# Performance work log

Hardware: AMD Instinct MI355X
Metric: run time of the kernel (lower is better)

## Reference

```python
import jax, jax.numpy as jnp
import numpy as np

CONV1_CH, CONV1_K = 8, 3
CONV2_CH, CONV2_K = 16, 2
DYN_POOL, MAX_POOL = 8, 4
FC1_IN, FC1_OUT = CONV2_CH * MAX_POOL * MAX_POOL, 100  # 256 -> 100


def k_max_pool(x, axis, k):
    # topk along axis, sort indices ascending, gather -> keeps original order of top-k
    xm = jnp.moveaxis(x, axis, -1)
    _, idx = jax.lax.top_k(xm, k)
    idx = jnp.sort(idx, axis=-1)
    out = jnp.take_along_axis(xm, idx, axis=-1)
    return jnp.moveaxis(out, -1, axis)


def _conv2d(x, w, b):
    y = jax.lax.conv_general_dilated(x, w, (1, 1), 'VALID',
                                     dimension_numbers=('NCHW', 'OIHW', 'NCHW'))
    return y + b[None, :, None, None]


def setup_inputs() -> dict:
    key = jax.random.key(0)
    ks = jax.random.split(key, 11)
    Lq, Ld, d, N = 128, 512, 64, 127
    inp = {
        'query': jax.random.normal(ks[0], (Lq, d), jnp.float32),
        'pos_doc': jax.random.normal(ks[1], (Ld, d), jnp.float32),
        'neg_docs': jax.random.normal(ks[2], (N, Ld, d), jnp.float32),
        'conv1_w': jax.random.normal(ks[3], (CONV1_CH, 1, CONV1_K, CONV1_K), jnp.float32) * 0.1,
        'conv1_b': jax.random.normal(ks[4], (CONV1_CH,), jnp.float32) * 0.1,
        'conv2_w': jax.random.normal(ks[5], (CONV2_CH, CONV1_CH, CONV2_K, CONV2_K), jnp.float32) * 0.1,
        'conv2_b': jax.random.normal(ks[6], (CONV2_CH,), jnp.float32) * 0.1,
        'lin1_w': jax.random.normal(ks[7], (FC1_OUT, FC1_IN), jnp.float32) * 0.05,
        'lin1_b': jax.random.normal(ks[8], (FC1_OUT,), jnp.float32) * 0.05,
        'lin2_w': jax.random.normal(ks[9], (1, FC1_OUT), jnp.float32) * 0.05,
        'lin2_b': jax.random.normal(ks[10], (1,), jnp.float32) * 0.05,
    }
    return inp


def reference(query, pos_doc, neg_docs, conv1_w, conv1_b, conv2_w, conv2_b,
              lin1_w, lin1_b, lin2_w, lin2_b):
    # Stack pos doc first, then negs (matches output stacking order in original)
    docs = jnp.concatenate([pos_doc[None], neg_docs], axis=0)      # [B, Ld, d]
    m = jnp.einsum('qd,bld->bql', query, docs)[:, None]            # [B, 1, Lq, Ld]
    # Layer 1: conv + relu + 2D k-max pooling to 8x8
    h = jax.nn.relu(_conv2d(m, conv1_w, conv1_b))                  # [B, 8, Lq-2, Ld-2]
    h = k_max_pool(h, 2, DYN_POOL)
    h = k_max_pool(h, 3, DYN_POOL)                                 # [B, 8, 8, 8]
    # Layer 2: conv + relu + 2D k-max pooling to 4x4
    h = jax.nn.relu(_conv2d(h, conv2_w, conv2_b))                  # [B, 16, 7, 7]
    h = k_max_pool(h, 2, MAX_POOL)
    h = k_max_pool(h, 3, MAX_POOL)                                 # [B, 16, 4, 4]
    feat = h.reshape(h.shape[0], -1)                               # [B, 256]
    z = jax.nn.relu(feat @ lin1_w.T + lin1_b)                      # [B, 100]
    s = jax.nn.relu(z @ lin2_w.T + lin2_b)                         # [B, 1]
    return s
```

## Files before the change

### kernel.cpp

```cpp
#include <hip/hip_runtime.h>
#include <cstdint>
#include <cstddef>

constexpr int kLq = 128;
constexpr int kLd = 512;
constexpr int kD  = 64;
constexpr int kB  = 128;
constexpr int kC1 = 8;
constexpr int kC2 = 16;
constexpr int kH1C = 510;
constexpr int kTileC = 51;
constexpr int kNTiles = 10;
constexpr int kMCols = 53;
constexpr int kNCand = kNTiles * 8;

constexpr int QT_PITCH = 132;
constexpr int DS_PITCH = 68;
constexpr int MS_PITCH = 57;

constexpr int kQtOff = 0;
constexpr int kDsOff = 64 * QT_PITCH;
constexpr int kMsOff = 0;
constexpr int kPsOff = kLq * MS_PITCH;
constexpr int kLdsFloats = kDsOff + 56 * DS_PITCH;

__device__ __forceinline__ uint64_t pack_key(float v, unsigned idx) {
  return ((uint64_t)__float_as_uint(v) << 32) | (uint32_t)(~idx);
}

template <int K>
__device__ __forceinline__ void topk_u64(uint64_t (&key)[K], uint64_t c) {
#pragma unroll
  for (int k = 0; k < K; ++k) {
    const bool g = c > key[k];
    const uint64_t hi = g ? c : key[k];
    c = g ? key[k] : c;
    key[k] = hi;
  }
}

template <int K, bool LEX>
__device__ __forceinline__ void topk_insert(float (&tv)[K], int (&ti)[K],
                                            float v, int idx) {
  bool gK = LEX ? ((v > tv[K - 1]) | ((v == tv[K - 1]) & (idx < ti[K - 1])))
                : (v > tv[K - 1]);
  if (!gK) return;
  bool g[K];
#pragma unroll
  for (int k = 0; k < K; ++k)
    g[k] = LEX ? ((v > tv[k]) | ((v == tv[k]) & (idx < ti[k]))) : (v > tv[k]);
#pragma unroll
  for (int k = K - 1; k >= 1; --k) {
    tv[k] = g[k - 1] ? tv[k - 1] : (g[k] ? v : tv[k]);
    ti[k] = g[k - 1] ? ti[k - 1] : (g[k] ? idx : ti[k]);
  }
  if (g[0]) { tv[0] = v; ti[0] = idx; }
}

__global__ __launch_bounds__(512, 6)
void convpool1_kernel(const float* __restrict__ query,
                      const float* __restrict__ pos_doc,
                      const float* __restrict__ neg_docs,
                      const float* __restrict__ c1w,
                      const float* __restrict__ c1b,
                      float* __restrict__ candv,
                      int* __restrict__ candi) {
  __shared__ float lds[kLdsFloats];
  float* q_t = lds + kQtOff;
  float* d_s = lds + kDsOff;
  float* m_s = lds + kMsOff;
  float* ps  = lds + kPsOff;

  const int tid  = threadIdx.x;
  const int tile = blockIdx.x;
  const int b    = blockIdx.y;
  const int l0g  = tile * kTileC;

  const float* doc =
      (b == 0) ? pos_doc : (neg_docs + (size_t)(b - 1) * kLd * kD);

  {
    const float4* qf4 = reinterpret_cast<const float4*>(query);
    for (int e = tid; e < (kLq * kD) / 4; e += 512) {
      const int q  = e & 127;
      const int f4 = e >> 7;
      const float4 v = qf4[q * 16 + f4];
      const int d0 = f4 << 2;
      q_t[(d0 + 0) * QT_PITCH + q] = v.x;
      q_t[(d0 + 1) * QT_PITCH + q] = v.y;
      q_t[(d0 + 2) * QT_PITCH + q] = v.z;
      q_t[(d0 + 3) * QT_PITCH + q] = v.w;
    }
  }
  for (int e = tid; e < 56 * 16; e += 512) {
    const int l  = e >> 4;
    const int d0 = (e & 15) << 2;
    float4 v = make_float4(0.f, 0.f, 0.f, 0.f);
    if (l < kMCols)
      v = reinterpret_cast<const float4*>(doc + (size_t)(l0g + l) * kD)[e & 15];
    *reinterpret_cast<float4*>(&d_s[l * DS_PITCH + d0]) = v;
  }
  __syncthreads();

  float acc[4][4] = {};
  if (tid < 32 * 14) {
    const int q0 = (tid & 31) << 2;
    const int l0 = (tid >> 5) << 2;
#pragma unroll 4
    for (int d = 0; d < kD; d += 4) {
      float4 qv[4];
#pragma unroll
      for (int j = 0; j < 4; ++j)
        qv[j] = *reinterpret_cast<const float4*>(&q_t[(d + j) * QT_PITCH + q0]);
      float4 dv[4];
#pragma unroll
      for (int li = 0; li < 4; ++li)
        dv[li] = *reinterpret_cast<const float4*>(&d_s[(l0 + li) * DS_PITCH + d]);
#pragma unroll
      for (int li = 0; li < 4; ++li) {
        const float4 w = dv[li];
        acc[0][li] += qv[0].x * w.x + qv[1].x * w.y + qv[2].x * w.z + qv[3].x * w.w;
        acc[1][li] += qv[0].y * w.x + qv[1].y * w.y + qv[2].y * w.z + qv[3].y * w.w;
        acc[2][li] += qv[0].z * w.x + qv[1].z * w.y + qv[2].z * w.z + qv[3].z * w.w;
        acc[3][li] += qv[0].w * w.x + qv[1].w * w.y + qv[2].w * w.z + qv[3].w * w.w;
      }
    }
  }
  __syncthreads();
  if (tid < 32 * 14) {
    const int q0 = (tid & 31) << 2;
    const int l0 = (tid >> 5) << 2;
#pragma unroll
    for (int qi = 0; qi < 4; ++qi)
#pragma unroll
      for (int li = 0; li < 4; ++li)
        m_s[(q0 + qi) * MS_PITCH + (l0 + li)] = acc[qi][li];
  }
  __syncthreads();

  if (tid < kC1 * kTileC) {
    const int c = tid / kTileC;
    const int j = tid % kTileC;
    float w[9];
#pragma unroll
    for (int k = 0; k < 9; ++k) w[k] = c1w[c * 9 + k];
    const float bias = c1b[c];

    uint64_t key[8];
#pragma unroll
    for (int k = 0; k < 8; ++k) key[k] = 0;

    float acc01 = 0.f, s0_pend = 0.f;
    for (int t = 0; t < kLq; ++t) {
      const float x0 = m_s[t * MS_PITCH + j];
      const float x1 = m_s[t * MS_PITCH + j + 1];
      const float x2 = m_s[t * MS_PITCH + j + 2];
      const float S0 = w[0] * x0 + w[1] * x1 + w[2] * x2;
      const float S1 = w[3] * x0 + w[4] * x1 + w[5] * x2;
      const float S2 = w[6] * x0 + w[7] * x1 + w[8] * x2;
      if (t >= 2) {
        const float v = fmaxf(bias + acc01 + S2, 0.f);
        topk_u64<8>(key, pack_key(v, (unsigned)(t - 2)));
      }
      acc01 = s0_pend + S1;
      s0_pend = S0;
    }
#pragma unroll
    for (int k = 0; k < 8; ++k) {
      const uint32_t lo_k = (uint32_t)key[k];
      int slot = 0;
#pragma unroll
      for (int m = 0; m < 8; ++m) slot += ((uint32_t)key[m] > lo_k);
      ps[(c * 8 + slot) * 52 + j] = __uint_as_float((uint32_t)(key[k] >> 32));
    }
  }
  __syncthreads();

  if (tid < 64) {
    const int g = tid;
    uint64_t key[8];
#pragma unroll
    for (int k = 0; k < 8; ++k) key[k] = 0;
    for (int j = 0; j < kTileC; ++j)
      topk_u64<8>(key, pack_key(ps[g * 52 + j], (unsigned)(l0g + j)));
    float* cv = candv + ((size_t)b * 64 + g) * kNCand + tile * 8;
    int*   ci = candi + ((size_t)b * 64 + g) * kNCand + tile * 8;
#pragma unroll
    for (int k = 0; k < 8; ++k) {
      const uint32_t lo_k = (uint32_t)key[k];
      int slot = 0;
#pragma unroll
      for (int m = 0; m < 8; ++m) slot += ((uint32_t)key[m] > lo_k);
      cv[slot] = __uint_as_float((uint32_t)(key[k] >> 32));
      ci[slot] = (int)(~lo_k);
    }
  }
}

__global__ __launch_bounds__(512)
void tail_kernel(const float* __restrict__ candv, const int* __restrict__ candi,
                 const float* __restrict__ c2w, const float* __restrict__ c2b,
                 const float* __restrict__ l1w, const float* __restrict__ l1b,
                 const float* __restrict__ l2w, const float* __restrict__ l2b,
                 float* __restrict__ out) {
  __shared__ float mv[64][8][8];
  __shared__ int   mi[64][8][8];
  __shared__ float w2s[kC2 * kC1 * 4];
  __shared__ float b2s[kC2];
  __shared__ float h2in[kC1][8][8];
  __shared__ float h2o[kC2][7][7];
  __shared__ float h3[kC2][4][7];
  __shared__ __align__(16) float feat[256];
  __shared__ float zbuf[100];

  const int b = blockIdx.x, tid = threadIdx.x;

  if (tid < kC2 * kC1 * 4) w2s[tid] = c2w[tid];
  if (tid < kC2) b2s[tid] = c2b[tid];

  const int g = tid >> 3, lane8 = tid & 7;
  float tv[8]; int ti[8];
#pragma unroll
  for (int k = 0; k < 8; ++k) { tv[k] = -1.f; ti[k] = 0x7fffffff; }
  {
    const float* cv = candv + ((size_t)b * 64 + g) * kNCand;
    const int*   ci = candi + ((size_t)b * 64 + g) * kNCand;
    for (int p = lane8; p < kNCand; p += 8)
      topk_insert<8, false>(tv, ti, cv[p], ci[p]);
#pragma unroll
    for (int k = 0; k < 8; ++k) { mv[g][lane8][k] = tv[k]; mi[g][lane8][k] = ti[k]; }
  }
  __syncthreads();

#pragma unroll
  for (int s = 4; s >= 1; s >>= 1) {
    if (lane8 < s) {
#pragma unroll
      for (int kk = 0; kk < 8; ++kk)
        topk_insert<8, true>(tv, ti, mv[g][lane8 + s][kk], mi[g][lane8 + s][kk]);
      if (s > 1) {
#pragma unroll
        for (int k = 0; k < 8; ++k) { mv[g][lane8][k] = tv[k]; mi[g][lane8][k] = ti[k]; }
      }
    }
    __syncthreads();
  }
  if (lane8 == 0) {
    const int c = g >> 3, row = g & 7;
#pragma unroll
    for (int k = 0; k < 8; ++k) {
      int slot = 0;
#pragma unroll
      for (int m = 0; m < 8; ++m) slot += (ti[m] < ti[k]);
      h2in[c][row][slot] = tv[k];
    }
  }
  __syncthreads();

  for (int v = tid; v < kC2 * 49; v += 512) {
    const int c2 = v / 49;
    const int r  = (v % 49) / 7;
    const int j  = v % 7;
    float s = b2s[c2];
#pragma unroll
    for (int cin = 0; cin < kC1; ++cin) {
      const float* wp = &w2s[(c2 * kC1 + cin) * 4];
      s += wp[0] * h2in[cin][r][j]     + wp[1] * h2in[cin][r][j + 1];
      s += wp[2] * h2in[cin][r + 1][j] + wp[3] * h2in[cin][r + 1][j + 1];
    }
    h2o[c2][r][j] = fmaxf(s, 0.f);
  }
  __syncthreads();

  if (tid < kC2 * 7) {
    const int c2 = tid / 7, j = tid % 7;
    float tv4[4]; int ti4[4];
#pragma unroll
    for (int k = 0; k < 4; ++k) { tv4[k] = -1.f; ti4[k] = 0x7fffffff; }
    for (int r = 0; r < 7; ++r) topk_insert<4, false>(tv4, ti4, h2o[c2][r][j], r);
#pragma unroll
    for (int k = 0; k < 4; ++k) {
      int slot = 0;
#pragma unroll
      for (int m = 0; m < 4; ++m) slot += (ti4[m] < ti4[k]);
      h3[c2][slot][j] = tv4[k];
    }
  }
  __syncthreads();

  if (tid < kC2 * 4) {
    const int c2 = tid >> 2, r = tid & 3;
    float tv4[4]; int ti4[4];
#pragma unroll
    for (int k = 0; k < 4; ++k) { tv4[k] = -1.f; ti4[k] = 0x7fffffff; }
    for (int j = 0; j < 7; ++j) topk_insert<4, false>(tv4, ti4, h3[c2][r][j], j);
#pragma unroll
    for (int k = 0; k < 4; ++k) {
      int slot = 0;
#pragma unroll
      for (int m = 0; m < 4; ++m) slot += (ti4[m] < ti4[k]);
      feat[c2 * 16 + r * 4 + slot] = tv4[k];
    }
  }
  __syncthreads();

  if (tid < 100) {
    const int o = tid;
    float s = l1b[o];
    const float4* wr = reinterpret_cast<const float4*>(l1w + (size_t)o * 256);
    const float4* fr = reinterpret_cast<const float4*>(feat);
    for (int i = 0; i < 64; ++i) {
      const float4 w = wr[i], f = fr[i];
      s += w.x * f.x + w.y * f.y + w.z * f.z + w.w * f.w;
    }
    zbuf[o] = fmaxf(s, 0.f);
  }
  __syncthreads();

  if (tid < 64) {
    float s = 0.f;
    for (int o = tid; o < 100; o += 64) s += zbuf[o] * l2w[o];
#pragma unroll
    for (int off = 32; off >= 1; off >>= 1) s += __shfl_down(s, off, 64);
    if (tid == 0) out[b] = fmaxf(s + l2b[0], 0.f);
  }
}

extern "C" void kernel_launch(void* const* d_in, const int* in_sizes, int n_in,
                              void* d_out, int out_size, void* d_ws,
                              size_t ws_size, hipStream_t stream) {
  const float* query    = (const float*)d_in[0];
  const float* pos_doc  = (const float*)d_in[1];
  const float* neg_docs = (const float*)d_in[2];
  const float* c1w      = (const float*)d_in[3];
  const float* c1b      = (const float*)d_in[4];
  const float* c2w      = (const float*)d_in[5];
  const float* c2b      = (const float*)d_in[6];
  const float* l1w      = (const float*)d_in[7];
  const float* l1b      = (const float*)d_in[8];
  const float* l2w      = (const float*)d_in[9];
  const float* l2b      = (const float*)d_in[10];
  float* out = (float*)d_out;

  float* candv = (float*)d_ws;
  int*   candi = (int*)((char*)d_ws + (size_t)kB * 64 * kNCand * sizeof(float));

  dim3 gridA(kNTiles, kB);
  hipLaunchKernelGGL(convpool1_kernel, gridA, dim3(512), 0, stream,
                     query, pos_doc, neg_docs, c1w, c1b, candv, candi);
  hipLaunchKernelGGL(tail_kernel, dim3(kB), dim3(512), 0, stream,
                     candv, candi, c2w, c2b, l1w, l1b, l2w, l2b, out);
}
```

Baseline: 268.7 us.

## Double block size and split conv1 row scan across thread pairs with LDS merge

The first kernel moves to 1024 threads per block. The matmul now gives each thread 2 query rows instead of 4. The conv1 top-k scan over 128 rows is split between two threads, each handling about half the rows, and their top-8 packed keys are merged through a new LDS buffer. The tail kernel swaps the float/index top-k insertion for packed u64 keys, loads the candidates into registers first, and splits the FC1 dot products across 4 lanes with shuffle reductions. The intent is more parallelism for the serial per-column scan, at the cost of higher register pressure per block, an extra sync, and more LDS use.

After: 273.6 us. No clear change (+1.8%).

```diff
diff --git a/kernel.cpp b/kernel.cpp
--- a/kernel.cpp
+++ b/kernel.cpp
@@ -8,11 +8,11 @@
 constexpr int kB  = 128;
 constexpr int kC1 = 8;
 constexpr int kC2 = 16;
-constexpr int kH1C = 510;
 constexpr int kTileC = 51;
 constexpr int kNTiles = 10;
 constexpr int kMCols = 53;
 constexpr int kNCand = kNTiles * 8;
+constexpr int kNPair = kC1 * kTileC;
 
 constexpr int QT_PITCH = 132;
 constexpr int DS_PITCH = 68;
@@ -21,8 +21,9 @@
 constexpr int kQtOff = 0;
 constexpr int kDsOff = 64 * QT_PITCH;
 constexpr int kMsOff = 0;
-constexpr int kPsOff = kLq * MS_PITCH;
-constexpr int kLdsFloats = kDsOff + 56 * DS_PITCH;
+constexpr int kPsOff = kDsOff;
+constexpr int kHkOff = kDsOff + 56 * DS_PITCH;
+constexpr int kLdsFloats = kHkOff + kNPair * 8 * 2;
 
 __device__ __forceinline__ uint64_t pack_key(float v, unsigned idx) {
   return ((uint64_t)__float_as_uint(v) << 32) | (uint32_t)(~idx);
@@ -39,25 +40,7 @@
   }
 }
 
-template <int K, bool LEX>
-__device__ __forceinline__ void topk_insert(float (&tv)[K], int (&ti)[K],
-                                            float v, int idx) {
-  bool gK = LEX ? ((v > tv[K - 1]) | ((v == tv[K - 1]) & (idx < ti[K - 1])))
-                : (v > tv[K - 1]);
-  if (!gK) return;
-  bool g[K];
-#pragma unroll
-  for (int k = 0; k < K; ++k)
-    g[k] = LEX ? ((v > tv[k]) | ((v == tv[k]) & (idx < ti[k]))) : (v > tv[k]);
-#pragma unroll
-  for (int k = K - 1; k >= 1; --k) {
-    tv[k] = g[k - 1] ? tv[k - 1] : (g[k] ? v : tv[k]);
-    ti[k] = g[k - 1] ? ti[k - 1] : (g[k] ? idx : ti[k]);
-  }
-  if (g[0]) { tv[0] = v; ti[0] = idx; }
-}
-
-__global__ __launch_bounds__(512, 6)
+__global__ __launch_bounds__(1024, 8)
 void convpool1_kernel(const float* __restrict__ query,
                       const float* __restrict__ pos_doc,
                       const float* __restrict__ neg_docs,
@@ -70,6 +53,7 @@
   float* d_s = lds + kDsOff;
   float* m_s = lds + kMsOff;
   float* ps  = lds + kPsOff;
+  uint64_t* hk = reinterpret_cast<uint64_t*>(lds + kHkOff);
 
   const int tid  = threadIdx.x;
   const int tile = blockIdx.x;
@@ -81,7 +65,7 @@
 
   {
     const float4* qf4 = reinterpret_cast<const float4*>(query);
-    for (int e = tid; e < (kLq * kD) / 4; e += 512) {
+    for (int e = tid; e < (kLq * kD) / 4; e += 1024) {
       const int q  = e & 127;
       const int f4 = e >> 7;
       const float4 v = qf4[q * 16 + f4];
@@ -92,26 +76,26 @@
       q_t[(d0 + 3) * QT_PITCH + q] = v.w;
     }
   }
-  for (int e = tid; e < 56 * 16; e += 512) {
-    const int l  = e >> 4;
-    const int d0 = (e & 15) << 2;
+  if (tid < 56 * 16) {
+    const int l  = tid >> 4;
+    const int d0 = (tid & 15) << 2;
     float4 v = make_float4(0.f, 0.f, 0.f, 0.f);
     if (l < kMCols)
-      v = reinterpret_cast<const float4*>(doc + (size_t)(l0g + l) * kD)[e & 15];
+      v = reinterpret_cast<const float4*>(doc + (size_t)(l0g + l) * kD)[tid & 15];
     *reinterpret_cast<float4*>(&d_s[l * DS_PITCH + d0]) = v;
   }
   __syncthreads();
 
-  float acc[4][4] = {};
-  if (tid < 32 * 14) {
-    const int q0 = (tid & 31) << 2;
-    const int l0 = (tid >> 5) << 2;
+  float acc[2][4] = {};
+  if (tid < 64 * 14) {
+    const int q0 = (tid & 63) << 1;
+    const int l0 = (tid >> 6) << 2;
 #pragma unroll 4
     for (int d = 0; d < kD; d += 4) {
-      float4 qv[4];
+      float2 qv[4];
 #pragma unroll
       for (int j = 0; j < 4; ++j)
-        qv[j] = *reinterpret_cast<const float4*>(&q_t[(d + j) * QT_PITCH + q0]);
+        qv[j] = *reinterpret_cast<const float2*>(&q_t[(d + j) * QT_PITCH + q0]);
       float4 dv[4];
 #pragma unroll
       for (int li = 0; li < 4; ++li)
@@ -121,50 +105,63 @@
         const float4 w = dv[li];
         acc[0][li] += qv[0].x * w.x + qv[1].x * w.y + qv[2].x * w.z + qv[3].x * w.w;
         acc[1][li] += qv[0].y * w.x + qv[1].y * w.y + qv[2].y * w.z + qv[3].y * w.w;
-        acc[2][li] += qv[0].z * w.x + qv[1].z * w.y + qv[2].z * w.z + qv[3].z * w.w;
-        acc[3][li] += qv[0].w * w.x + qv[1].w * w.y + qv[2].w * w.z + qv[3].w * w.w;
       }
     }
   }
   __syncthreads();
-  if (tid < 32 * 14) {
-    const int q0 = (tid & 31) << 2;
-    const int l0 = (tid >> 5) << 2;
-#pragma unroll
-    for (int qi = 0; qi < 4; ++qi)
+  if (tid < 64 * 14) {
+    const int q0 = (tid & 63) << 1;
+    const int l0 = (tid >> 6) << 2;
+#pragma unroll
+    for (int qi = 0; qi < 2; ++qi)
 #pragma unroll
       for (int li = 0; li < 4; ++li)
         m_s[(q0 + qi) * MS_PITCH + (l0 + li)] = acc[qi][li];
   }
   __syncthreads();
 
-  if (tid < kC1 * kTileC) {
-    const int c = tid / kTileC;
-    const int j = tid % kTileC;
+  const int h    = tid & 1;
+  const int pair = tid >> 1;
+  uint64_t key[8];
+#pragma unroll
+  for (int k = 0; k < 8; ++k) key[k] = 0;
+  if (pair < kNPair) {
+    const int c = pair / kTileC;
+    const int j = pair % kTileC;
     float w[9];
 #pragma unroll
     for (int k = 0; k < 9; ++k) w[k] = c1w[c * 9 + k];
     const float bias = c1b[c];
-
-    uint64_t key[8];
-#pragma unroll
-    for (int k = 0; k < 8; ++k) key[k] = 0;
+    const int tBase = h ? 63 : 0;
 
     float acc01 = 0.f, s0_pend = 0.f;
-    for (int t = 0; t < kLq; ++t) {
+    for (int s = 0; s < 65; ++s) {
+      const int t = tBase + s;
       const float x0 = m_s[t * MS_PITCH + j];
       const float x1 = m_s[t * MS_PITCH + j + 1];
       const float x2 = m_s[t * MS_PITCH + j + 2];
       const float S0 = w[0] * x0 + w[1] * x1 + w[2] * x2;
       const float S1 = w[3] * x0 + w[4] * x1 + w[5] * x2;
       const float S2 = w[6] * x0 + w[7] * x1 + w[8] * x2;
-      if (t >= 2) {
+      if (s >= 2) {
         const float v = fmaxf(bias + acc01 + S2, 0.f);
         topk_u64<8>(key, pack_key(v, (unsigned)(t - 2)));
       }
       acc01 = s0_pend + S1;
       s0_pend = S0;
     }
+    if (h == 1) {
+#pragma unroll
+      for (int k = 0; k < 8; ++k) hk[pair * 8 + k] = key[k];
+    }
+  }
+  __syncthreads();
+
+  if (pair < kNPair && h == 0) {
+    const int c = pair / kTileC;
+    const int j = pair % kTileC;
+#pragma unroll
+    for (int k = 0; k < 8; ++k) topk_u64<8>(key, hk[pair * 8 + k]);
 #pragma unroll
     for (int k = 0; k < 8; ++k) {
       const uint32_t lo_k = (uint32_t)key[k];
@@ -178,20 +175,20 @@
 
   if (tid < 64) {
     const int g = tid;
-    uint64_t key[8];
-#pragma unroll
-    for (int k = 0; k < 8; ++k) key[k] = 0;
+    uint64_t ck[8];
+#pragma unroll
+    for (int k = 0; k < 8; ++k) ck[k] = 0;
     for (int j = 0; j < kTileC; ++j)
-      topk_u64<8>(key, pack_key(ps[g * 52 + j], (unsigned)(l0g + j)));
+      topk_u64<8>(ck, pack_key(ps[g * 52 + j], (unsigned)(l0g + j)));
     float* cv = candv + ((size_t)b * 64 + g) * kNCand + tile * 8;
     int*   ci = candi + ((size_t)b * 64 + g) * kNCand + tile * 8;
 #pragma unroll
     for (int k = 0; k < 8; ++k) {
-      const uint32_t lo_k = (uint32_t)key[k];
-      int slot = 0;
-#pragma unroll
-      for (int m = 0; m < 8; ++m) slot += ((uint32_t)key[m] > lo_k);
-      cv[slot] = __uint_as_float((uint32_t)(key[k] >> 32));
+      const uint32_t lo_k = (uint32_t)ck[k];
+      int slot = 0;
+#pragma unroll
+      for (int m = 0; m < 8; ++m) slot += ((uint32_t)ck[m] > lo_k);
+      cv[slot] = __uint_as_float((uint32_t)(ck[k] >> 32));
       ci[slot] = (int)(~lo_k);
     }
   }
@@ -203,8 +200,7 @@
                  const float* __restrict__ l1w, const float* __restrict__ l1b,
                  const float* __restrict__ l2w, const float* __restrict__ l2b,
                  float* __restrict__ out) {
-  __shared__ float mv[64][8][8];
-  __shared__ int   mi[64][8][8];
+  __shared__ uint64_t mk[64][8][8];
   __shared__ float w2s[kC2 * kC1 * 4];
   __shared__ float b2s[kC2];
   __shared__ float h2in[kC1][8][8];
@@ -219,16 +215,23 @@
   if (tid < kC2) b2s[tid] = c2b[tid];
 
   const int g = tid >> 3, lane8 = tid & 7;
-  float tv[8]; int ti[8];
-#pragma unroll
-  for (int k = 0; k < 8; ++k) { tv[k] = -1.f; ti[k] = 0x7fffffff; }
+  uint64_t key[8];
+#pragma unroll
+  for (int k = 0; k < 8; ++k) key[k] = 0;
   {
     const float* cv = candv + ((size_t)b * 64 + g) * kNCand;
     const int*   ci = candi + ((size_t)b * 64 + g) * kNCand;
-    for (int p = lane8; p < kNCand; p += 8)
-      topk_insert<8, false>(tv, ti, cv[p], ci[p]);
-#pragma unroll
-    for (int k = 0; k < 8; ++k) { mv[g][lane8][k] = tv[k]; mi[g][lane8][k] = ti[k]; }
+    float cvr[10]; int cir[10];
+#pragma unroll
+    for (int it = 0; it < 10; ++it) {
+      cvr[it] = cv[lane8 + it * 8];
+      cir[it] = ci[lane8 + it * 8];
+    }
+#pragma unroll
+    for (int it = 0; it < 10; ++it)
+      topk_u64<8>(key, pack_key(cvr[it], (unsigned)cir[it]));
+#pragma unroll
+    for (int k = 0; k < 8; ++k) mk[g][lane8][k] = key[k];
   }
   __syncthreads();
 
@@ -237,10 +240,10 @@
     if (lane8 < s) {
 #pragma unroll
       for (int kk = 0; kk < 8; ++kk)
-        topk_insert<8, true>(tv, ti, mv[g][lane8 + s][kk], mi[g][lane8 + s][kk]);
+        topk_u64<8>(key, mk[g][lane8 + s][kk]);
       if (s > 1) {
 #pragma unroll
-        for (int k = 0; k < 8; ++k) { mv[g][lane8][k] = tv[k]; mi[g][lane8][k] = ti[k]; }
+        for (int k = 0; k < 8; ++k) mk[g][lane8][k] = key[k];
       }
     }
     __syncthreads();
@@ -249,10 +252,11 @@
     const int c = g >> 3, row = g & 7;
 #pragma unroll
     for (int k = 0; k < 8; ++k) {
-      int slot = 0;
-#pragma unroll
-      for (int m = 0; m < 8; ++m) slot += (ti[m] < ti[k]);
-      h2in[c][row][slot] = tv[k];
+      const uint32_t lo_k = (uint32_t)key[k];
+      int slot = 0;
+#pragma unroll
+      for (int m = 0; m < 8; ++m) slot += ((uint32_t)key[m] > lo_k);
+      h2in[c][row][slot] = __uint_as_float((uint32_t)(key[k] >> 32));
     }
   }
   __syncthreads();
@@ -274,46 +278,51 @@
 
   if (tid < kC2 * 7) {
     const int c2 = tid / 7, j = tid % 7;
-    float tv4[4]; int ti4[4];
-#pragma unroll
-    for (int k = 0; k < 4; ++k) { tv4[k] = -1.f; ti4[k] = 0x7fffffff; }
-    for (int r = 0; r < 7; ++r) topk_insert<4, false>(tv4, ti4, h2o[c2][r][j], r);
+    uint64_t k4[4];
+#pragma unroll
+    for (int k = 0; k < 4; ++k) k4[k] = 0;
+    for (int r = 0; r < 7; ++r) topk_u64<4>(k4, pack_key(h2o[c2][r][j], (unsigned)r));
 #pragma unroll
     for (int k = 0; k < 4; ++k) {
-      int slot = 0;
-#pragma unroll
-      for (int m = 0; m < 4; ++m) slot += (ti4[m] < ti4[k]);
-      h3[c2][slot][j] = tv4[k];
+      const uint32_t lo_k = (uint32_t)k4[k];
+      int slot = 0;
+#pragma unroll
+      for (int m = 0; m < 4; ++m) slot += ((uint32_t)k4[m] > lo_k);
+      h3[c2][slot][j] = __uint_as_float((uint32_t)(k4[k] >> 32));
     }
   }
   __syncthreads();
 
   if (tid < kC2 * 4) {
     const int c2 = tid >> 2, r = tid & 3;
-    float tv4[4]; int ti4[4];
-#pragma unroll
-    for (int k = 0; k < 4; ++k) { tv4[k] = -1.f; ti4[k] = 0x7fffffff; }
-    for (int j = 0; j < 7; ++j) topk_insert<4, false>(tv4, ti4, h3[c2][r][j], j);
+    uint64_t k4[4];
+#pragma unroll
+    for (int k = 0; k < 4; ++k) k4[k] = 0;
+    for (int j = 0; j < 7; ++j) topk_u64<4>(k4, pack_key(h3[c2][r][j], (unsigned)j));
 #pragma unroll
     for (int k = 0; k < 4; ++k) {
-      int slot = 0;
-#pragma unroll
-      for (int m = 0; m < 4; ++m) slot += (ti4[m] < ti4[k]);
-      feat[c2 * 16 + r * 4 + slot] = tv4[k];
-    }
-  }
-  __syncthreads();
-
-  if (tid < 100) {
-    const int o = tid;
-    float s = l1b[o];
-    const float4* wr = reinterpret_cast<const float4*>(l1w + (size_t)o * 256);
-    const float4* fr = reinterpret_cast<const float4*>(feat);
-    for (int i = 0; i < 64; ++i) {
+      const uint32_t lo_k = (uint32_t)k4[k];
+      int slot = 0;
+#pragma unroll
+      for (int m = 0; m < 4; ++m) slot += ((uint32_t)k4[m] > lo_k);
+      feat[c2 * 16 + r * 4 + slot] = __uint_as_float((uint32_t)(k4[k] >> 32));
+    }
+  }
+  __syncthreads();
+
+  if (tid < 400) {
+    const int o = tid >> 2, part = tid & 3;
+    const float4* wr = reinterpret_cast<const float4*>(l1w + (size_t)o * 256) + part * 16;
+    const float4* fr = reinterpret_cast<const float4*>(feat) + part * 16;
+    float s = 0.f;
+#pragma unroll
+    for (int i = 0; i < 16; ++i) {
       const float4 w = wr[i], f = fr[i];
       s += w.x * f.x + w.y * f.y + w.z * f.z + w.w * f.w;
     }
-    zbuf[o] = fmaxf(s, 0.f);
+    s += __shfl_xor(s, 1, 64);
+    s += __shfl_xor(s, 2, 64);
+    if (part == 0) zbuf[o] = fmaxf(s + l1b[o], 0.f);
   }
   __syncthreads();
 
@@ -346,7 +355,7 @@
   int*   candi = (int*)((char*)d_ws + (size_t)kB * 64 * kNCand * sizeof(float));
 
   dim3 gridA(kNTiles, kB);
-  hipLaunchKernelGGL(convpool1_kernel, gridA, dim3(512), 0, stream,
+  hipLaunchKernelGGL(convpool1_kernel, gridA, dim3(1024), 0, stream,
                      query, pos_doc, neg_docs, c1w, c1b, candv, candi);
   hipLaunchKernelGGL(tail_kernel, dim3(kB), dim3(512), 0, stream,
                      candv, candi, c2w, c2b, l1w, l1b, l2w, l2b, out);
```
